# Kernel optimization log

Hardware: AMD Instinct MI355X
Metric: run time of the kernel (lower is better)

The kernel has to match this reference:

```python
import jax, jax.numpy as jnp
import numpy as np

B, S, HID = 2, 2048, 2048
H, HKV, D = 32, 8, 128


def _rope(x, cos, sin):
    # x: [B, S, n_heads, D]; cos/sin: [S, D], only first D//2 columns used.
    half = x.shape[-1] // 2
    x0, x1 = x[..., :half], x[..., half:]
    c = cos[None, :, None, :half]
    s = sin[None, :, None, :half]
    return jnp.concatenate([x0 * c - x1 * s, x0 * s + x1 * c], axis=-1)


def setup_inputs() -> dict:
    key = jax.random.key(0)
    ks = jax.random.split(key, 7)
    return {
        "hidden_states": jax.random.normal(ks[0], (B, S, HID), jnp.float32),
        "sin_table": jax.random.uniform(ks[1], (S, D), jnp.float32),
        "cos_table": jax.random.uniform(ks[2], (S, D), jnp.float32),
        "Wq": jax.random.normal(ks[3], (HID, H * D), jnp.float32) * 0.02,
        "Wk": jax.random.normal(ks[4], (HID, HKV * D), jnp.float32) * 0.02,
        "Wv": jax.random.normal(ks[5], (HID, HKV * D), jnp.float32) * 0.02,
        "Wo": jax.random.normal(ks[6], (H * D, HID), jnp.float32) * 0.02,
    }


def reference(hidden_states, sin_table, cos_table, Wq, Wk, Wv, Wo):
    b, s, _ = hidden_states.shape
    q = (hidden_states @ Wq).reshape(b, s, H, D)
    k = (hidden_states @ Wk).reshape(b, s, HKV, D)
    v = (hidden_states @ Wv).reshape(b, s, HKV, D)

    q = _rope(q, cos_table, sin_table)
    k = _rope(k, cos_table, sin_table)

    q = q.transpose(0, 2, 1, 3)  # [B, H, S, D]
    k = k.transpose(0, 2, 1, 3)  # [B, HKV, S, D]
    v = v.transpose(0, 2, 1, 3)

    g = H // HKV
    k = jnp.repeat(k, g, axis=1)  # [B, H, S, D]
    v = jnp.repeat(v, g, axis=1)

    scale = 1.0 / np.sqrt(D).astype(np.float32)
    scores = jnp.einsum("bhqd,bhkd->bhqk", q, k) * scale
    causal = jnp.tril(jnp.ones((s, s), dtype=bool))
    scores = jnp.where(causal, scores, -jnp.inf)
    attn = jax.nn.softmax(scores, axis=-1)
    out = jnp.einsum("bhqk,bhkd->bhqd", attn, v)  # [B, H, S, D]
    out = out.transpose(0, 2, 1, 3).reshape(b, s, H * D)
    return out @ Wo
```

## Files before the change

kernel.cpp:

```cpp
#include <hip/hip_runtime.h>
#include <hip/hip_bf16.h>
#include <math.h>

#define BB 2
#define SS 2048
#define HID 2048
#define NH 32
#define NKV 8
#define DD 128

typedef unsigned short u16;
typedef __attribute__((ext_vector_type(8))) short short8;
typedef __attribute__((ext_vector_type(4))) float f32x4;
typedef __attribute__((ext_vector_type(16))) float f32x16;
typedef __attribute__((ext_vector_type(4))) unsigned short us4;

__device__ __forceinline__ u16 f2bf(float f) {
    unsigned int u = __float_as_uint(f);
    u += 0x7fff + ((u >> 16) & 1);
    return (u16)(u >> 16);
}
__device__ __forceinline__ float bf2f(u16 h) {
    return __uint_as_float(((unsigned int)h) << 16);
}

#define GLOAD16(gp, lp) __builtin_amdgcn_global_load_lds(                      \
    (const __attribute__((address_space(1))) void*)(gp),                       \
    (__attribute__((address_space(3))) void*)(lp), 16, 0, 0)

#define MFMA32(a, b, c) __builtin_amdgcn_mfma_f32_32x32x16_bf16(a, b, c, 0, 0, 0)

__global__ __launch_bounds__(256) void cvt_k(const float* __restrict__ in,
                                             u16* __restrict__ out, int n8)
{
    int i = blockIdx.x * 256 + threadIdx.x;
    if (i >= n8) return;
    f32x4 a = ((const f32x4*)in)[i * 2];
    f32x4 b = ((const f32x4*)in)[i * 2 + 1];
    short8 o;
#pragma unroll
    for (int j = 0; j < 4; ++j) { o[j] = (short)f2bf(a[j]); o[4 + j] = (short)f2bf(b[j]); }
    ((short8*)out)[i] = o;
}

__global__ __launch_bounds__(256) void tw_k(const float* __restrict__ in,
                                            u16* __restrict__ out, int R, int C)
{
    __shared__ float t[32][33];
    const int tc = blockIdx.x * 32, tr = blockIdx.y * 32;
    const int r = threadIdx.x >> 3, c4 = (threadIdx.x & 7) * 4;
    f32x4 v = *(const f32x4*)(in + (size_t)(tr + r) * C + tc + c4);
#pragma unroll
    for (int j = 0; j < 4; ++j) t[r][c4 + j] = v[j];
    __syncthreads();
    us4 o;
#pragma unroll
    for (int j = 0; j < 4; ++j) o[j] = f2bf(t[c4 + j][r]);
    *(us4*)(out + (size_t)(tc + r) * R + tr + c4) = o;
}

__global__ __launch_bounds__(256) void vtr_k(const u16* __restrict__ Vb,
                                             u16* __restrict__ Vt)
{
    __shared__ u16 t[64][72];
    const int s0 = blockIdx.x * 64, d0 = blockIdx.y * 64;
    const int b = blockIdx.z >> 3, hkv = blockIdx.z & 7;
    const int tid = threadIdx.x;
    const int rr = tid >> 3, cc = (tid & 7) * 8;
#pragma unroll
    for (int it = 0; it < 2; ++it) {
        int row = rr + it * 32;
        short8 v = *(const short8*)(Vb + ((size_t)(b * SS + s0 + row) * NKV + hkv) * DD + d0 + cc);
#pragma unroll
        for (int j = 0; j < 8; ++j) t[row][cc + j] = (u16)v[j];
    }
    __syncthreads();
#pragma unroll
    for (int it = 0; it < 2; ++it) {
        int dr = rr + it * 32;
        short8 o;
#pragma unroll
        for (int j = 0; j < 8; ++j) o[j] = (short)t[cc + j][dr];
        *(short8*)(Vt + ((size_t)(b * NKV + hkv) * DD + d0 + dr) * SS + s0 + cc) = o;
    }
}

__global__ __launch_bounds__(256) void gemmqkv_k(const u16* __restrict__ A,
                                                 const u16* __restrict__ Wcat,
                                                 u16* __restrict__ Qb_,
                                                 u16* __restrict__ Kb_,
                                                 u16* __restrict__ Vt_)
{
    const int K = HID;
    const int swz = (blockIdx.x & 7) * 192 + ((int)blockIdx.x >> 3);
    const int bx = swz % 48, by = swz / 48;
    const int m0 = by * 128, n0 = bx * 128;

    __shared__ u16 Al[128 * 64];
    __shared__ u16 Bl[128 * 64];
    const int tid = threadIdx.x;
    const int lane = tid & 63, w = tid >> 6;
    const int lo = lane & 15, hi = lane >> 4;
    const int wm = w >> 1, wn = w & 1;

    const int srow = w * 32 + (lane >> 3);
    const int sslot = (lane & 7) ^ (lane >> 3);
    const u16* Asrc = A + (size_t)(m0 + srow) * K + sslot * 8;
    const u16* Bsrc = Wcat + (size_t)(n0 + srow) * K + sslot * 8;

    f32x4 acc[4][4] = {};

    for (int k0 = 0; k0 < K; k0 += 64) {
        __syncthreads();
#pragma unroll
        for (int t = 0; t < 4; ++t) {
            GLOAD16(Asrc + (size_t)t * 8 * K + k0, &Al[(w * 32 + t * 8) * 64]);
            GLOAD16(Bsrc + (size_t)t * 8 * K + k0, &Bl[(w * 32 + t * 8) * 64]);
        }
        __syncthreads();
#pragma unroll
        for (int c = 0; c < 2; ++c) {
            short8 af[4], bfv[4];
#pragma unroll
            for (int i = 0; i < 4; ++i) {
                int row = wm * 64 + i * 16 + lo;
                af[i] = *(const short8*)&Al[row * 64 + (((c * 4 + hi) ^ (lo & 7)) * 8)];
            }
#pragma unroll
            for (int j = 0; j < 4; ++j) {
                int row = wn * 64 + j * 16 + lo;
                bfv[j] = *(const short8*)&Bl[row * 64 + (((c * 4 + hi) ^ (lo & 7)) * 8)];
            }
#pragma unroll
            for (int i = 0; i < 4; ++i)
#pragma unroll
                for (int j = 0; j < 4; ++j)
                    acc[i][j] = __builtin_amdgcn_mfma_f32_16x16x32_bf16(af[i], bfv[j], acc[i][j], 0, 0, 0);
        }
    }

    if (n0 >= 5120) {
        const int cn0 = n0 - 5120;
#pragma unroll
        for (int i = 0; i < 4; ++i) {
            int gm = m0 + wm * 64 + i * 16 + hi * 4;
            int bb = gm >> 11, s = gm & (SS - 1);
#pragma unroll
            for (int j = 0; j < 4; ++j) {
                int gn = cn0 + wn * 64 + j * 16 + lo;
                int hkv = gn >> 7, d = gn & 127;
                us4 o;
#pragma unroll
                for (int r = 0; r < 4; ++r) o[r] = f2bf(acc[i][j][r]);
                *(us4*)(Vt_ + (((size_t)(bb * NKV + hkv) * DD + d) * SS + s)) = o;
            }
        }
    } else {
        u16* Cb;
        int cstride, cn0;
        if (n0 < 4096) { Cb = Qb_; cstride = NH * DD;  cn0 = n0; }
        else           { Cb = Kb_; cstride = NKV * DD; cn0 = n0 - 4096; }
#pragma unroll
        for (int i = 0; i < 4; ++i) {
            int gm = m0 + wm * 64 + i * 16 + hi * 4;
#pragma unroll
            for (int j = 0; j < 4; ++j) {
                int gn = cn0 + wn * 64 + j * 16 + lo;
#pragma unroll
                for (int r = 0; r < 4; ++r)
                    Cb[(size_t)(gm + r) * cstride + gn] = f2bf(acc[i][j][r]);
            }
        }
    }
}

template<bool C_F32>
__global__ __launch_bounds__(256) void gemm2s_k(const u16* __restrict__ A,
                                                const u16* __restrict__ Bt,
                                                void* __restrict__ Cp,
                                                int M, int N, int K, int nbx)
{
    const int cpx = (int)gridDim.x >> 3;
    const int swz = (blockIdx.x & 7) * cpx + ((int)blockIdx.x >> 3);
    const int bx = swz % nbx, by = swz / nbx;
    const int m0 = by * 128, n0 = bx * 128;

    __shared__ u16 Al[128 * 64];
    __shared__ u16 Bl[128 * 64];
    const int tid = threadIdx.x;
    const int lane = tid & 63, w = tid >> 6;
    const int lo = lane & 15, hi = lane >> 4;
    const int wm = w >> 1, wn = w & 1;

    const int srow = w * 32 + (lane >> 3);
    const int sslot = (lane & 7) ^ (lane >> 3);
    const u16* Asrc = A + (size_t)(m0 + srow) * K + sslot * 8;
    const u16* Bsrc = Bt + (size_t)(n0 + srow) * K + sslot * 8;

    f32x4 acc[4][4] = {};

    for (int k0 = 0; k0 < K; k0 += 64) {
        __syncthreads();
#pragma unroll
        for (int t = 0; t < 4; ++t) {
            GLOAD16(Asrc + (size_t)t * 8 * K + k0, &Al[(w * 32 + t * 8) * 64]);
            GLOAD16(Bsrc + (size_t)t * 8 * K + k0, &Bl[(w * 32 + t * 8) * 64]);
        }
        __syncthreads();
#pragma unroll
        for (int c = 0; c < 2; ++c) {
            short8 af[4], bfv[4];
#pragma unroll
            for (int i = 0; i < 4; ++i) {
                int row = wm * 64 + i * 16 + lo;
                af[i] = *(const short8*)&Al[row * 64 + (((c * 4 + hi) ^ (lo & 7)) * 8)];
            }
#pragma unroll
            for (int j = 0; j < 4; ++j) {
                int row = wn * 64 + j * 16 + lo;
                bfv[j] = *(const short8*)&Bl[row * 64 + (((c * 4 + hi) ^ (lo & 7)) * 8)];
            }
#pragma unroll
            for (int i = 0; i < 4; ++i)
#pragma unroll
                for (int j = 0; j < 4; ++j)
                    acc[i][j] = __builtin_amdgcn_mfma_f32_16x16x32_bf16(af[i], bfv[j], acc[i][j], 0, 0, 0);
        }
    }

#pragma unroll
    for (int i = 0; i < 4; ++i) {
        int gm = m0 + wm * 64 + i * 16 + hi * 4;
#pragma unroll
        for (int j = 0; j < 4; ++j) {
            int gn = n0 + wn * 64 + j * 16 + lo;
#pragma unroll
            for (int r = 0; r < 4; ++r) {
                if constexpr (C_F32)
                    ((float*)Cp)[(size_t)(gm + r) * N + gn] = acc[i][j][r];
                else
                    ((u16*)Cp)[(size_t)(gm + r) * N + gn] = f2bf(acc[i][j][r]);
            }
        }
    }
}

__global__ __launch_bounds__(256) void rope_k(u16* buf,
                                              const float* __restrict__ cosT,
                                              const float* __restrict__ sinT,
                                              int nheads, float scale)
{
    int idx = blockIdx.x * 256 + threadIdx.x;
    int total = BB * SS * nheads * 64;
    if (idx >= total) return;
    int d = idx & 63;
    int rem = idx >> 6;
    int hh = rem % nheads;
    int s = (rem / nheads) & (SS - 1);
    int bb = rem / (nheads * SS);
    size_t base = ((size_t)(bb * SS + s) * nheads + hh) * DD;
    float x0 = bf2f(buf[base + d]), x1 = bf2f(buf[base + d + 64]);
    float c = cosT[s * DD + d], sn = sinT[s * DD + d];
    buf[base + d]      = f2bf((x0 * c - x1 * sn) * scale);
    buf[base + d + 64] = f2bf((x0 * sn + x1 * c) * scale);
}

__device__ __forceinline__ short8 make_pa(float p0, float p1, float p2, float p3,
                                          float p4, float p5, float p6, float p7,
                                          int hi1)
{
    unsigned w0, w1, w2, w3;
    asm("v_cvt_pk_bf16_f32 %0, %1, %2" : "=v"(w0) : "v"(p0), "v"(p1));
    asm("v_cvt_pk_bf16_f32 %0, %1, %2" : "=v"(w1) : "v"(p2), "v"(p3));
    asm("v_cvt_pk_bf16_f32 %0, %1, %2" : "=v"(w2) : "v"(p4), "v"(p5));
    asm("v_cvt_pk_bf16_f32 %0, %1, %2" : "=v"(w3) : "v"(p6), "v"(p7));
    unsigned xw0 = (unsigned)__shfl_xor((int)w0, 32);
    unsigned xw1 = (unsigned)__shfl_xor((int)w1, 32);
    unsigned xw2 = (unsigned)__shfl_xor((int)w2, 32);
    unsigned xw3 = (unsigned)__shfl_xor((int)w3, 32);
    union { unsigned u[4]; short8 s; } cv;
    cv.u[0] = hi1 ? xw2 : w0;
    cv.u[1] = hi1 ? xw3 : w1;
    cv.u[2] = hi1 ? w2 : xw0;
    cv.u[3] = hi1 ? w3 : xw1;
    return cv.s;
}

__global__ __launch_bounds__(512, 2) void attn9_k(const u16* __restrict__ Qb,
                                                  const u16* __restrict__ Kb,
                                                  const u16* __restrict__ Vt,
                                                  u16* __restrict__ AO)
{
    const int wgid = blockIdx.x;
    const int k = wgid & 7;
    const int j = wgid >> 3;
    const int u = j & 31, v = j >> 5;
    const int qtb = u >> 3;
    const int qt = v ? 7 - qtb : qtb;
    const int h  = (k & 3) * 8 + (u & 7);
    const int b  = k >> 2;
    const int hkv = h >> 2;
    const int tid = threadIdx.x;
    const int w = tid >> 6, lane = tid & 63;
    const int l31 = lane & 31, hi1 = lane >> 5;
    const int qr0 = qt * 256 + w * 32;

    __shared__ u16 Kl[2][64 * 128];
    __shared__ u16 Vl[2][128 * 64];

    short8 qf[8];
    {
        const u16* qrow = Qb + ((size_t)(b * SS + qr0 + l31) * NH + h) * DD + hi1 * 8;
#pragma unroll
        for (int ks = 0; ks < 8; ++ks) qf[ks] = *(const short8*)(qrow + ks * 16);
    }

    const u16* kbase = Kb + ((size_t)b * SS * NKV + hkv) * DD;
    const u16* vbase = Vt + (size_t)(b * NKV + hkv) * DD * SS;

    f32x16 oacc[4] = {};
    float mreg = -INFINITY, lreg = 0.f;

    const int nkt = 4 * qt + 4;
    const int rk = lane >> 4, sk = lane & 15;
    const int rv = lane >> 3, sv = lane & 7;

#pragma unroll
    for (int i = 0; i < 2; ++i) {
        const int c = w * 2 + i;
        const int krow = c * 4 + rk;
        GLOAD16(kbase + (size_t)krow * (NKV * DD) + ((sk ^ (krow & 15)) * 8), &Kl[0][c * 512]);
        const int vrow = c * 8 + rv;
        GLOAD16(vbase + (size_t)vrow * SS + ((sv ^ (vrow & 7)) * 8), &Vl[0][c * 512]);
    }
    __syncthreads();

    int buf = 0;
    for (int kt = 0; kt < nkt; ++kt) {
        const int kv0 = kt * 64;
        if (kt + 1 < nkt) {
            const int kv1 = kv0 + 64;
#pragma unroll
            for (int i = 0; i < 2; ++i) {
                const int c = w * 2 + i;
                const int krow = c * 4 + rk;
                GLOAD16(kbase + (size_t)(kv1 + krow) * (NKV * DD) + ((sk ^ (krow & 15)) * 8),
                        &Kl[buf ^ 1][c * 512]);
                const int vrow = c * 8 + rv;
                GLOAD16(vbase + (size_t)vrow * SS + kv1 + ((sv ^ (vrow & 7)) * 8),
                        &Vl[buf ^ 1][c * 512]);
            }
        }

        if (kv0 <= qr0 + 31) {
            const u16* Kc = Kl[buf];
            const u16* Vc = Vl[buf];

            f32x16 s0 = {}, s1 = {};
            __builtin_amdgcn_s_setprio(1);
#pragma unroll
            for (int ks = 0; ks < 8; ++ks) {
                const int slot = (((2 * ks + hi1) ^ sk) * 8);
                short8 kf0 = *(const short8*)&Kc[l31 * 128 + slot];
                s0 = MFMA32(kf0, qf[ks], s0);
                short8 kf1 = *(const short8*)&Kc[(32 + l31) * 128 + slot];
                s1 = MFMA32(kf1, qf[ks], s1);
            }
            __builtin_amdgcn_s_setprio(0);

            const int qab = qr0 + l31;
            if (kv0 + 63 > qr0) {
#pragma unroll
                for (int r = 0; r < 16; ++r) {
                    const int off = (r & 3) + 8 * (r >> 2) + 4 * hi1;
                    if (kv0 + off > qab)      s0[r] = -INFINITY;
                    if (kv0 + 32 + off > qab) s1[r] = -INFINITY;
                }
            }
            float m0 = fmaxf(s0[0], s1[0]), m1 = fmaxf(s0[1], s1[1]);
            float m2 = fmaxf(s0[2], s1[2]), m3 = fmaxf(s0[3], s1[3]);
#pragma unroll
            for (int r = 4; r < 16; r += 4) {
                m0 = fmaxf(m0, fmaxf(s0[r],     s1[r]));
                m1 = fmaxf(m1, fmaxf(s0[r + 1], s1[r + 1]));
                m2 = fmaxf(m2, fmaxf(s0[r + 2], s1[r + 2]));
                m3 = fmaxf(m3, fmaxf(s0[r + 3], s1[r + 3]));
            }
            float mx = fmaxf(fmaxf(m0, m1), fmaxf(m2, m3));
            mx = fmaxf(mx, __shfl_xor(mx, 32));

            if (__any(mx > mreg + 8.0f)) {
                const float nm = fmaxf(mreg, mx);
                const float al = exp2f(mreg - nm);
                mreg = nm;
                lreg *= al;
#pragma unroll
                for (int r = 0; r < 16; ++r) {
                    const float ar = __shfl(al, (r & 3) + 8 * (r >> 2) + 4 * hi1);
#pragma unroll
                    for (int db = 0; db < 4; ++db) oacc[db][r] *= ar;
                }
            }

#pragma unroll
            for (int r = 0; r < 16; ++r) {
                s0[r] = exp2f(s0[r] - mreg);
                s1[r] = exp2f(s1[r] - mreg);
            }
            float sa = 0.f, sb = 0.f, sc_ = 0.f, sd = 0.f;
#pragma unroll
            for (int r = 0; r < 16; r += 4) {
                sa  += s0[r]     + s1[r];
                sb  += s0[r + 1] + s1[r + 1];
                sc_ += s0[r + 2] + s1[r + 2];
                sd  += s0[r + 3] + s1[r + 3];
            }
            lreg += (sa + sb) + (sc_ + sd);

            short8 pa0 = make_pa(s0[0], s0[1], s0[2],  s0[3],  s0[4],  s0[5],  s0[6],  s0[7],  hi1);
            short8 pa1 = make_pa(s0[8], s0[9], s0[10], s0[11], s0[12], s0[13], s0[14], s0[15], hi1);
            short8 pa2 = make_pa(s1[0], s1[1], s1[2],  s1[3],  s1[4],  s1[5],  s1[6],  s1[7],  hi1);
            short8 pa3 = make_pa(s1[8], s1[9], s1[10], s1[11], s1[12], s1[13], s1[14], s1[15], hi1);

            __builtin_amdgcn_s_setprio(1);
#pragma unroll
            for (int db = 0; db < 4; ++db) {
                const int vr = (db * 32 + l31) * 64;
                short8 vf0 = *(const short8*)&Vc[vr + (((0 + hi1) ^ sv) * 8)];
                oacc[db] = MFMA32(pa0, vf0, oacc[db]);
                short8 vf1 = *(const short8*)&Vc[vr + (((2 + hi1) ^ sv) * 8)];
                oacc[db] = MFMA32(pa1, vf1, oacc[db]);
                short8 vf2 = *(const short8*)&Vc[vr + (((4 + hi1) ^ sv) * 8)];
                oacc[db] = MFMA32(pa2, vf2, oacc[db]);
                short8 vf3 = *(const short8*)&Vc[vr + (((6 + hi1) ^ sv) * 8)];
                oacc[db] = MFMA32(pa3, vf3, oacc[db]);
            }
            __builtin_amdgcn_s_setprio(0);
        }
        __syncthreads();
        buf ^= 1;
    }

    const float lf = lreg + __shfl_xor(lreg, 32);
#pragma unroll
    for (int r = 0; r < 16; ++r) {
        const int qrw = (r & 3) + 8 * (r >> 2) + 4 * hi1;
        const float linv = 1.0f / __shfl(lf, qrw);
        u16* orow = AO + ((size_t)(b * SS + qr0 + qrw) * NH + h) * DD + l31;
#pragma unroll
        for (int db = 0; db < 4; ++db)
            orow[db * 32] = f2bf(oacc[db][r] * linv);
    }
}

template<bool A_BF16, bool C_F32>
__global__ __launch_bounds__(256) void gemm_k(const void* __restrict__ Ap,
                                              const float* __restrict__ Bp,
                                              void* __restrict__ Cp,
                                              int M, int N, int K)
{
    __shared__ u16 Asm[128 * 40];
    __shared__ u16 Bsm[128 * 40];
    const int tid  = threadIdx.x;
    const int lane = tid & 63, wid = tid >> 6;
    const int lo = lane & 15, hi = lane >> 4;
    const int wm = wid >> 1, wn = wid & 1;
    const int m0 = blockIdx.y * 128, n0 = blockIdx.x * 128;
    f32x4 acc[4][4] = {};
    const int nkt = K >> 5;
    for (int kt = 0; kt < nkt; ++kt) {
        const int k0 = kt << 5;
        __syncthreads();
        if constexpr (A_BF16) {
            const u16* A = (const u16*)Ap;
#pragma unroll
            for (int it = 0; it < 4; ++it) {
                int f = it * 256 + tid;
                int row = f >> 3, kg = (f & 7) * 4;
                us4 v = *(const us4*)(A + (size_t)(m0 + row) * K + k0 + kg);
#pragma unroll
                for (int j = 0; j < 4; ++j) Asm[row * 40 + kg + j] = v[j];
            }
        } else {
            const float* A = (const float*)Ap;
#pragma unroll
            for (int it = 0; it < 4; ++it) {
                int f = it * 256 + tid;
                int row = f >> 3, kg = (f & 7) * 4;
                f32x4 v = *(const f32x4*)(A + (size_t)(m0 + row) * K + k0 + kg);
#pragma unroll
                for (int j = 0; j < 4; ++j) Asm[row * 40 + kg + j] = f2bf(v[j]);
            }
        }
#pragma unroll
        for (int it = 0; it < 4; ++it) {
            int f = it * 256 + tid;
            int kr = f >> 5, cg = (f & 31) * 4;
            f32x4 v = *(const f32x4*)(Bp + (size_t)(k0 + kr) * N + n0 + cg);
#pragma unroll
            for (int j = 0; j < 4; ++j) Bsm[(cg + j) * 40 + kr] = f2bf(v[j]);
        }
        __syncthreads();
        short8 af[4], bfr[4];
#pragma unroll
        for (int i = 0; i < 4; ++i)
            af[i] = *(const short8*)&Asm[(wm * 64 + i * 16 + lo) * 40 + hi * 8];
#pragma unroll
        for (int j = 0; j < 4; ++j)
            bfr[j] = *(const short8*)&Bsm[(wn * 64 + j * 16 + lo) * 40 + hi * 8];
#pragma unroll
        for (int i = 0; i < 4; ++i)
#pragma unroll
            for (int j = 0; j < 4; ++j)
                acc[i][j] = __builtin_amdgcn_mfma_f32_16x16x32_bf16(af[i], bfr[j], acc[i][j], 0, 0, 0);
    }
#pragma unroll
    for (int i = 0; i < 4; ++i) {
        int gm = m0 + wm * 64 + i * 16 + hi * 4;
#pragma unroll
        for (int j = 0; j < 4; ++j) {
            int gn = n0 + wn * 64 + j * 16 + lo;
#pragma unroll
            for (int r = 0; r < 4; ++r) {
                if constexpr (C_F32)
                    ((float*)Cp)[(size_t)(gm + r) * N + gn] = acc[i][j][r];
                else
                    ((u16*)Cp)[(size_t)(gm + r) * N + gn] = f2bf(acc[i][j][r]);
            }
        }
    }
}

__global__ __launch_bounds__(64) void attn_k(const u16* __restrict__ Qb,
                                             const u16* __restrict__ Kb,
                                             const u16* __restrict__ Vb,
                                             u16* __restrict__ AO)
{
    const int blk = blockIdx.x;
    const int qt = blk & (SS / 16 - 1);
    const int h  = (blk >> 7) & (NH - 1);
    const int b  = blk >> 12;
    const int hkv = h >> 2;
    const int lane = threadIdx.x;
    const int lo = lane & 15, hi = lane >> 4;
    const int qbase = qt * 16;
    __shared__ float sc[16][32];
    __shared__ u16 vt[128 * 40];
    short8 qf[4];
    const u16* qrow = Qb + ((size_t)(b * SS + qbase + lo) * NH + h) * DD;
#pragma unroll
    for (int c = 0; c < 4; ++c) qf[c] = *(const short8*)(qrow + c * 32 + hi * 8);
    f32x4 oacc[8] = {};
    float m[4] = {-INFINITY, -INFINITY, -INFINITY, -INFINITY};
    float l[4] = {0.f, 0.f, 0.f, 0.f};
    const int nkt = (qbase + 16 + 31) >> 5;
    for (int kt = 0; kt < nkt; ++kt) {
        const int kv0 = kt << 5;
        f32x4 s0 = {}, s1 = {};
        const u16* kb0 = Kb + ((size_t)(b * SS + kv0) * NKV + hkv) * DD;
#pragma unroll
        for (int c = 0; c < 4; ++c) {
            short8 k0f = *(const short8*)(kb0 + (size_t)lo * (NKV * DD) + c * 32 + hi * 8);
            short8 k1f = *(const short8*)(kb0 + (size_t)(lo + 16) * (NKV * DD) + c * 32 + hi * 8);
            s0 = __builtin_amdgcn_mfma_f32_16x16x32_bf16(qf[c], k0f, s0, 0, 0, 0);
            s1 = __builtin_amdgcn_mfma_f32_16x16x32_bf16(qf[c], k1f, s1, 0, 0, 0);
        }
#pragma unroll
        for (int i = 0; i < 8; ++i) {
            int g = i * 64 + lane;
            int row = g >> 4, dg = (g & 15) * 8;
            short8 vv = *(const short8*)(Vb + ((size_t)(b * SS + kv0 + row) * NKV + hkv) * DD + dg);
#pragma unroll
            for (int j = 0; j < 8; ++j) vt[(dg + j) * 40 + row] = (u16)vv[j];
        }
        float alpha[4];
#pragma unroll
        for (int r = 0; r < 4; ++r) {
            int qrowi = qbase + hi * 4 + r;
            float v0 = s0[r]; if (kv0 + lo > qrowi)      v0 = -INFINITY;
            float v1 = s1[r]; if (kv0 + 16 + lo > qrowi) v1 = -INFINITY;
            float mx = fmaxf(v0, v1);
#pragma unroll
            for (int off = 1; off < 16; off <<= 1) mx = fmaxf(mx, __shfl_xor(mx, off, 64));
            float nm = fmaxf(m[r], mx);
            float a = __expf(m[r] - nm);
            v0 = __expf(v0 - nm);
            v1 = __expf(v1 - nm);
            float ps = v0 + v1;
#pragma unroll
            for (int off = 1; off < 16; off <<= 1) ps += __shfl_xor(ps, off, 64);
            l[r] = l[r] * a + ps;
            m[r] = nm;
            alpha[r] = a;
            sc[hi * 4 + r][lo] = v0;
            sc[hi * 4 + r][16 + lo] = v1;
        }
#pragma unroll
        for (int n = 0; n < 8; ++n)
#pragma unroll
            for (int r = 0; r < 4; ++r) oacc[n][r] *= alpha[r];
        __syncthreads();
        f32x4 p0 = *(const f32x4*)&sc[lo][hi * 8];
        f32x4 p1 = *(const f32x4*)&sc[lo][hi * 8 + 4];
        short8 pf;
#pragma unroll
        for (int j = 0; j < 4; ++j) {
            pf[j]     = (short)f2bf(p0[j]);
            pf[4 + j] = (short)f2bf(p1[j]);
        }
#pragma unroll
        for (int n = 0; n < 8; ++n) {
            short8 vf = *(const short8*)&vt[(n * 16 + lo) * 40 + hi * 8];
            oacc[n] = __builtin_amdgcn_mfma_f32_16x16x32_bf16(pf, vf, oacc[n], 0, 0, 0);
        }
        __syncthreads();
    }
#pragma unroll
    for (int n = 0; n < 8; ++n) {
#pragma unroll
        for (int r = 0; r < 4; ++r) {
            size_t idx = ((size_t)(b * SS + qbase + hi * 4 + r) * NH + h) * DD + n * 16 + lo;
            AO[idx] = f2bf(oacc[n][r] / l[r]);
        }
    }
}

extern "C" void kernel_launch(void* const* d_in, const int* in_sizes, int n_in,
                              void* d_out, int out_size, void* d_ws, size_t ws_size,
                              hipStream_t stream) {
    const float* hs   = (const float*)d_in[0];
    const float* sinT = (const float*)d_in[1];
    const float* cosT = (const float*)d_in[2];
    const float* Wq   = (const float*)d_in[3];
    const float* Wk   = (const float*)d_in[4];
    const float* Wv   = (const float*)d_in[5];
    const float* Wo   = (const float*)d_in[6];
    float* out = (float*)d_out;
    const int M = BB * SS;
    u16* ws = (u16*)d_ws;

    const size_t NEED = 109051904;
    if (ws_size >= NEED) {
        u16* Qb   = ws;
        u16* Kb   = ws + 16777216;
        u16* Vt   = ws + 25165824;
        u16* Wcat = ws + 29360128;
        u16* hsb  = ws + 41943040;
        u16* Wot  = Wcat;
        u16* AO   = ws + 37748736;

        cvt_k<<<4096, 256, 0, stream>>>(hs, hsb, (M * HID) / 8);
        tw_k<<<dim3(4096 / 32, 2048 / 32), 256, 0, stream>>>(Wq, Wcat, HID, NH * DD);
        tw_k<<<dim3(1024 / 32, 2048 / 32), 256, 0, stream>>>(Wk, Wcat + (size_t)4096 * 2048, HID, NKV * DD);
        tw_k<<<dim3(1024 / 32, 2048 / 32), 256, 0, stream>>>(Wv, Wcat + (size_t)5120 * 2048, HID, NKV * DD);

        gemmqkv_k<<<1536, 256, 0, stream>>>(hsb, Wcat, Qb, Kb, Vt);

        rope_k<<<(BB * SS * NH * 64 + 255) / 256, 256, 0, stream>>>(Qb, cosT, sinT, NH, 0.12751744f);
        rope_k<<<(BB * SS * NKV * 64 + 255) / 256, 256, 0, stream>>>(Kb, cosT, sinT, NKV, 1.0f);
        tw_k<<<dim3(2048 / 32, 4096 / 32), 256, 0, stream>>>(Wo, Wot, NH * DD, HID);

        attn9_k<<<SS / 256 * NH * BB, 512, 0, stream>>>(Qb, Kb, Vt, AO);

        gemm2s_k<true><<<512, 256, 0, stream>>>(AO, Wot, out, M, HID, NH * DD, HID / 128);
    } else {
        u16* Qb   = ws;
        u16* Kbuf = Qb   + (size_t)BB * SS * NH * DD;
        u16* Vbuf = Kbuf + (size_t)BB * SS * NKV * DD;
        u16* AO   = Vbuf + (size_t)BB * SS * NKV * DD;

        gemm_k<false, false><<<dim3((NH * DD) / 128, M / 128), 256, 0, stream>>>(hs, Wq, Qb, M, NH * DD, HID);
        gemm_k<false, false><<<dim3((NKV * DD) / 128, M / 128), 256, 0, stream>>>(hs, Wk, Kbuf, M, NKV * DD, HID);
        gemm_k<false, false><<<dim3((NKV * DD) / 128, M / 128), 256, 0, stream>>>(hs, Wv, Vbuf, M, NKV * DD, HID);
        rope_k<<<(BB * SS * NH * 64 + 255) / 256, 256, 0, stream>>>(Qb, cosT, sinT, NH, 0.08838834764831845f);
        rope_k<<<(BB * SS * NKV * 64 + 255) / 256, 256, 0, stream>>>(Kbuf, cosT, sinT, NKV, 1.0f);
        attn_k<<<BB * NH * (SS / 16), 64, 0, stream>>>(Qb, Kbuf, Vbuf, AO);
        gemm_k<true, true><<<dim3(HID / 128, M / 128), 256, 0, stream>>>(AO, Wo, out, M, HID, NH * DD);
    }
}
```

Baseline: 358.2 us.

## Replace QKV GEMM with 256x256-tile, 8-wave, double-buffered pipelined kernel

Replaces the 128x128 single-buffered QKV projection GEMM with a 256x256-tile kernel that uses 8 waves and two LDS stages, each holding two 128-row halves for A and B. Global-to-LDS loads for tile T+2 are issued partway through the MFMA work on tile T, using explicit vmcnt waits, barriers, sched_barrier and setprio raised around the MFMA runs. The aim is to overlap memory traffic with matrix math, raise arithmetic intensity per tile and remove the load-then-compute stall of the old loop. In exchange it uses 128 KB of LDS per block and more accumulator registers, and the hand-written wait counts and barriers are fragile. The other MFMA calls are only renamed to a macro.

```diff
diff --git a/kernel.cpp b/kernel.cpp
--- a/kernel.cpp
+++ b/kernel.cpp
@@ -29,6 +29,7 @@
     (__attribute__((address_space(3))) void*)(lp), 16, 0, 0)
 
 #define MFMA32(a, b, c) __builtin_amdgcn_mfma_f32_32x32x16_bf16(a, b, c, 0, 0, 0)
+#define MFMA16(a, b, c) __builtin_amdgcn_mfma_f32_16x16x32_bf16(a, b, c, 0, 0, 0)
 
 __global__ __launch_bounds__(256) void cvt_k(const float* __restrict__ in,
                                              u16* __restrict__ out, int n8)
@@ -85,15 +86,168 @@
     }
 }
 
-__global__ __launch_bounds__(256) void gemmqkv_k(const u16* __restrict__ A,
-                                                 const u16* __restrict__ Wcat,
-                                                 u16* __restrict__ Qb_,
-                                                 u16* __restrict__ Kb_,
-                                                 u16* __restrict__ Vt_)
+__global__ __launch_bounds__(512, 2) void gemm8qkv_k(const u16* __restrict__ A,
+                                                     const u16* __restrict__ Bt,
+                                                     u16* __restrict__ Qb_,
+                                                     u16* __restrict__ Kb_,
+                                                     u16* __restrict__ Vt_)
 {
     const int K = HID;
-    const int swz = (blockIdx.x & 7) * 192 + ((int)blockIdx.x >> 3);
-    const int bx = swz % 48, by = swz / 48;
+    const int k8 = blockIdx.x & 7;
+    const int j  = (int)blockIdx.x >> 3;
+    const int bx = j >> 1, by = k8 * 2 + (j & 1);
+    const int m0 = by * 256, n0 = bx * 256;
+
+    __shared__ u16 Asl[4][128 * 64];
+    __shared__ u16 Bsl[4][128 * 64];
+
+    const int tid = threadIdx.x;
+    const int w = tid >> 6, lane = tid & 63;
+    const int wm = w >> 2, wn = w & 3;
+    const int lo = lane & 15, hi = lane >> 4;
+    const int brow0 = (wn & 1) * 64;
+
+    const int srow8 = lane >> 3;
+    const int skk = ((lane & 7) ^ srow8) * 8;
+    const u16* As = A + (size_t)(m0 + w * 16 + srow8) * K + skk;
+    const u16* Bs = Bt + (size_t)(n0 + w * 16 + srow8) * K + skk;
+
+#define SA8(slot, half, kof) do {                                                        \
+    GLOAD16(As + (size_t)((half) * 128) * K + (kof), &Asl[slot][(w * 16) * 64]);         \
+    GLOAD16(As + (size_t)((half) * 128 + 8) * K + (kof), &Asl[slot][(w * 16 + 8) * 64]); \
+  } while (0)
+#define SB8(slot, half, kof) do {                                                        \
+    GLOAD16(Bs + (size_t)((half) * 128) * K + (kof), &Bsl[slot][(w * 16) * 64]);         \
+    GLOAD16(Bs + (size_t)((half) * 128 + 8) * K + (kof), &Bsl[slot][(w * 16 + 8) * 64]); \
+  } while (0)
+#define PHASE_END() do {                                       \
+    asm volatile("s_waitcnt lgkmcnt(0)" ::: "memory");         \
+    __builtin_amdgcn_sched_barrier(0);                         \
+    __builtin_amdgcn_s_barrier();                              \
+  } while (0)
+
+    f32x4 acc[8][4] = {};
+    const int nt = K >> 6;
+
+    SA8(0, 0, 0);  SA8(1, 1, 0);  SB8(0, 0, 0);  SB8(1, 1, 0);
+    SA8(2, 0, 64); SA8(3, 1, 64); SB8(2, 0, 64); SB8(3, 1, 64);
+    asm volatile("s_waitcnt vmcnt(8)" ::: "memory");
+    __builtin_amdgcn_s_barrier();
+
+#define TILE8(P, T) do {                                                                 \
+    const u16* Apan = Asl[(P) * 2 + wm];                                                 \
+    const u16* Bpan = Bsl[(P) * 2 + (wn >> 1)];                                          \
+    short8 afr[2][8]; short8 bfr[2][4];                                                  \
+                    \
+    _Pragma("unroll") for (int c = 0; c < 2; ++c) {                                      \
+      _Pragma("unroll") for (int i = 0; i < 4; ++i)                                      \
+        afr[c][i] = *(const short8*)&Apan[(i * 16 + lo) * 64 + (((c * 4 + hi) ^ (lo & 7)) * 8)]; \
+      _Pragma("unroll") for (int jj = 0; jj < 2; ++jj)                                   \
+        bfr[c][jj] = *(const short8*)&Bpan[(brow0 + jj * 16 + lo) * 64 + (((c * 4 + hi) ^ (lo & 7)) * 8)]; \
+    }                                                                                    \
+    __builtin_amdgcn_s_setprio(1);                                                       \
+    _Pragma("unroll") for (int i = 0; i < 4; ++i)                                        \
+      _Pragma("unroll") for (int jj = 0; jj < 2; ++jj) {                                 \
+        acc[i][jj] = MFMA16(afr[0][i], bfr[0][jj], acc[i][jj]);                          \
+        acc[i][jj] = MFMA16(afr[1][i], bfr[1][jj], acc[i][jj]);                          \
+      }                                                                                  \
+    __builtin_amdgcn_s_setprio(0);                                                       \
+    PHASE_END();                                                                         \
+                          \
+    _Pragma("unroll") for (int c = 0; c < 2; ++c) {                                      \
+      _Pragma("unroll") for (int i = 4; i < 8; ++i)                                      \
+        afr[c][i] = *(const short8*)&Apan[(i * 16 + lo) * 64 + (((c * 4 + hi) ^ (lo & 7)) * 8)]; \
+      _Pragma("unroll") for (int jj = 2; jj < 4; ++jj)                                   \
+        bfr[c][jj] = *(const short8*)&Bpan[(brow0 + jj * 16 + lo) * 64 + (((c * 4 + hi) ^ (lo & 7)) * 8)]; \
+    }                                                                                    \
+    __builtin_amdgcn_s_setprio(1);                                                       \
+    _Pragma("unroll") for (int i = 0; i < 4; ++i)                                        \
+      _Pragma("unroll") for (int jj = 2; jj < 4; ++jj) {                                 \
+        acc[i][jj] = MFMA16(afr[0][i], bfr[0][jj], acc[i][jj]);                          \
+        acc[i][jj] = MFMA16(afr[1][i], bfr[1][jj], acc[i][jj]);                          \
+      }                                                                                  \
+    __builtin_amdgcn_s_setprio(0);                                                       \
+    PHASE_END();                                                                         \
+                          \
+    __builtin_amdgcn_s_setprio(1);                                                       \
+    _Pragma("unroll") for (int i = 4; i < 8; ++i)                                        \
+      _Pragma("unroll") for (int jj = 0; jj < 2; ++jj) {                                 \
+        acc[i][jj] = MFMA16(afr[0][i], bfr[0][jj], acc[i][jj]);                          \
+        acc[i][jj] = MFMA16(afr[1][i], bfr[1][jj], acc[i][jj]);                          \
+      }                                                                                  \
+    __builtin_amdgcn_s_setprio(0);                                                       \
+    if ((T) + 2 < nt) {                                                                  \
+      SA8((P) * 2 + 0, 0, ((T) + 2) * 64); SA8((P) * 2 + 1, 1, ((T) + 2) * 64);          \
+    }                                                                                    \
+    PHASE_END();                                                                         \
+           \
+    __builtin_amdgcn_s_setprio(1);                                                       \
+    _Pragma("unroll") for (int i = 4; i < 8; ++i)                                        \
+      _Pragma("unroll") for (int jj = 2; jj < 4; ++jj) {                                 \
+        acc[i][jj] = MFMA16(afr[0][i], bfr[0][jj], acc[i][jj]);                          \
+        acc[i][jj] = MFMA16(afr[1][i], bfr[1][jj], acc[i][jj]);                          \
+      }                                                                                  \
+    __builtin_amdgcn_s_setprio(0);                                                       \
+    if ((T) + 2 < nt) {                                                                  \
+      SB8((P) * 2 + 0, 0, ((T) + 2) * 64); SB8((P) * 2 + 1, 1, ((T) + 2) * 64);          \
+      asm volatile("s_waitcnt vmcnt(8)" ::: "memory");                                   \
+    } else {                                                                             \
+      asm volatile("s_waitcnt vmcnt(0)" ::: "memory");                                   \
+    }                                                                                    \
+    asm volatile("s_waitcnt lgkmcnt(0)" ::: "memory");                                   \
+    __builtin_amdgcn_sched_barrier(0);                                                   \
+    __builtin_amdgcn_s_barrier();                                                        \
+  } while (0)
+
+    for (int T = 0; T < nt; T += 2) {
+        TILE8(0, T);
+        TILE8(1, T + 1);
+    }
+#undef TILE8
+
+    if (n0 >= 5120) {
+#pragma unroll
+        for (int i = 0; i < 8; ++i) {
+            int gm = m0 + wm * 128 + i * 16 + hi * 4;
+            int bb = gm >> 11, s = gm & (SS - 1);
+#pragma unroll
+            for (int jj = 0; jj < 4; ++jj) {
+                int gn = (n0 - 5120) + wn * 64 + jj * 16 + lo;
+                int hkv = gn >> 7, d = gn & 127;
+                us4 o;
+#pragma unroll
+                for (int r = 0; r < 4; ++r) o[r] = f2bf(acc[i][jj][r]);
+                *(us4*)(Vt_ + (((size_t)(bb * NKV + hkv) * DD + d) * SS + s)) = o;
+            }
+        }
+    } else {
+        u16* Cb;
+        int cstride, cn0;
+        if (n0 < 4096) { Cb = Qb_; cstride = NH * DD;  cn0 = n0; }
+        else           { Cb = Kb_; cstride = NKV * DD; cn0 = n0 - 4096; }
+#pragma unroll
+        for (int i = 0; i < 8; ++i) {
+            int gm = m0 + wm * 128 + i * 16 + hi * 4;
+#pragma unroll
+            for (int jj = 0; jj < 4; ++jj) {
+                int gn = cn0 + wn * 64 + jj * 16 + lo;
+#pragma unroll
+                for (int r = 0; r < 4; ++r)
+                    Cb[(size_t)(gm + r) * cstride + gn] = f2bf(acc[i][jj][r]);
+            }
+        }
+    }
+}
+
+template<bool C_F32>
+__global__ __launch_bounds__(256) void gemm2s_k(const u16* __restrict__ A,
+                                                const u16* __restrict__ Bt,
+                                                void* __restrict__ Cp,
+                                                int M, int N, int K, int nbx)
+{
+    const int cpx = (int)gridDim.x >> 3;
+    const int swz = (blockIdx.x & 7) * cpx + ((int)blockIdx.x >> 3);
+    const int bx = swz % nbx, by = swz / nbx;
     const int m0 = by * 128, n0 = bx * 128;
 
     __shared__ u16 Al[128 * 64];
@@ -106,7 +260,7 @@
     const int srow = w * 32 + (lane >> 3);
     const int sslot = (lane & 7) ^ (lane >> 3);
     const u16* Asrc = A + (size_t)(m0 + srow) * K + sslot * 8;
-    const u16* Bsrc = Wcat + (size_t)(n0 + srow) * K + sslot * 8;
+    const u16* Bsrc = Bt + (size_t)(n0 + srow) * K + sslot * 8;
 
     f32x4 acc[4][4] = {};
 
@@ -135,96 +289,7 @@
             for (int i = 0; i < 4; ++i)
 #pragma unroll
                 for (int j = 0; j < 4; ++j)
-                    acc[i][j] = __builtin_amdgcn_mfma_f32_16x16x32_bf16(af[i], bfv[j], acc[i][j], 0, 0, 0);
-        }
-    }
-
-    if (n0 >= 5120) {
-        const int cn0 = n0 - 5120;
-#pragma unroll
-        for (int i = 0; i < 4; ++i) {
-            int gm = m0 + wm * 64 + i * 16 + hi * 4;
-            int bb = gm >> 11, s = gm & (SS - 1);
-#pragma unroll
-            for (int j = 0; j < 4; ++j) {
-                int gn = cn0 + wn * 64 + j * 16 + lo;
-                int hkv = gn >> 7, d = gn & 127;
-                us4 o;
-#pragma unroll
-                for (int r = 0; r < 4; ++r) o[r] = f2bf(acc[i][j][r]);
-                *(us4*)(Vt_ + (((size_t)(bb * NKV + hkv) * DD + d) * SS + s)) = o;
-            }
-        }
-    } else {
-        u16* Cb;
-        int cstride, cn0;
-        if (n0 < 4096) { Cb = Qb_; cstride = NH * DD;  cn0 = n0; }
-        else           { Cb = Kb_; cstride = NKV * DD; cn0 = n0 - 4096; }
-#pragma unroll
-        for (int i = 0; i < 4; ++i) {
-            int gm = m0 + wm * 64 + i * 16 + hi * 4;
-#pragma unroll
-            for (int j = 0; j < 4; ++j) {
-                int gn = cn0 + wn * 64 + j * 16 + lo;
-#pragma unroll
-                for (int r = 0; r < 4; ++r)
-                    Cb[(size_t)(gm + r) * cstride + gn] = f2bf(acc[i][j][r]);
-            }
-        }
-    }
-}
-
-template<bool C_F32>
-__global__ __launch_bounds__(256) void gemm2s_k(const u16* __restrict__ A,
-                                                const u16* __restrict__ Bt,
-                                                void* __restrict__ Cp,
-                                                int M, int N, int K, int nbx)
-{
-    const int cpx = (int)gridDim.x >> 3;
-    const int swz = (blockIdx.x & 7) * cpx + ((int)blockIdx.x >> 3);
-    const int bx = swz % nbx, by = swz / nbx;
-    const int m0 = by * 128, n0 = bx * 128;
-
-    __shared__ u16 Al[128 * 64];
-    __shared__ u16 Bl[128 * 64];
-    const int tid = threadIdx.x;
-    const int lane = tid & 63, w = tid >> 6;
-    const int lo = lane & 15, hi = lane >> 4;
-    const int wm = w >> 1, wn = w & 1;
-
-    const int srow = w * 32 + (lane >> 3);
-    const int sslot = (lane & 7) ^ (lane >> 3);
-    const u16* Asrc = A + (size_t)(m0 + srow) * K + sslot * 8;
-    const u16* Bsrc = Bt + (size_t)(n0 + srow) * K + sslot * 8;
-
-    f32x4 acc[4][4] = {};
-
-    for (int k0 = 0; k0 < K; k0 += 64) {
-        __syncthreads();
-#pragma unroll
-        for (int t = 0; t < 4; ++t) {
-            GLOAD16(Asrc + (size_t)t * 8 * K + k0, &Al[(w * 32 + t * 8) * 64]);
-            GLOAD16(Bsrc + (size_t)t * 8 * K + k0, &Bl[(w * 32 + t * 8) * 64]);
-        }
-        __syncthreads();
-#pragma unroll
-        for (int c = 0; c < 2; ++c) {
-            short8 af[4], bfv[4];
-#pragma unroll
-            for (int i = 0; i < 4; ++i) {
-                int row = wm * 64 + i * 16 + lo;
-                af[i] = *(const short8*)&Al[row * 64 + (((c * 4 + hi) ^ (lo & 7)) * 8)];
-            }
-#pragma unroll
-            for (int j = 0; j < 4; ++j) {
-                int row = wn * 64 + j * 16 + lo;
-                bfv[j] = *(const short8*)&Bl[row * 64 + (((c * 4 + hi) ^ (lo & 7)) * 8)];
-            }
-#pragma unroll
-            for (int i = 0; i < 4; ++i)
-#pragma unroll
-                for (int j = 0; j < 4; ++j)
-                    acc[i][j] = __builtin_amdgcn_mfma_f32_16x16x32_bf16(af[i], bfv[j], acc[i][j], 0, 0, 0);
+                    acc[i][j] = MFMA16(af[i], bfv[j], acc[i][j]);
         }
     }
 
@@ -512,7 +577,7 @@
         for (int i = 0; i < 4; ++i)
 #pragma unroll
             for (int j = 0; j < 4; ++j)
-                acc[i][j] = __builtin_amdgcn_mfma_f32_16x16x32_bf16(af[i], bfr[j], acc[i][j], 0, 0, 0);
+                acc[i][j] = MFMA16(af[i], bfr[j], acc[i][j]);
     }
 #pragma unroll
     for (int i = 0; i < 4; ++i) {
@@ -562,8 +627,8 @@
         for (int c = 0; c < 4; ++c) {
             short8 k0f = *(const short8*)(kb0 + (size_t)lo * (NKV * DD) + c * 32 + hi * 8);
             short8 k1f = *(const short8*)(kb0 + (size_t)(lo + 16) * (NKV * DD) + c * 32 + hi * 8);
-            s0 = __builtin_amdgcn_mfma_f32_16x16x32_bf16(qf[c], k0f, s0, 0, 0, 0);
-            s1 = __builtin_amdgcn_mfma_f32_16x16x32_bf16(qf[c], k1f, s1, 0, 0, 0);
+            s0 = MFMA16(qf[c], k0f, s0);
+            s1 = MFMA16(qf[c], k1f, s1);
         }
 #pragma unroll
         for (int i = 0; i < 8; ++i) {
@@ -611,7 +676,7 @@
 #pragma unroll
         for (int n = 0; n < 8; ++n) {
             short8 vf = *(const short8*)&vt[(n * 16 + lo) * 40 + hi * 8];
-            oacc[n] = __builtin_amdgcn_mfma_f32_16x16x32_bf16(pf, vf, oacc[n], 0, 0, 0);
+            oacc[n] = MFMA16(pf, vf, oacc[n]);
         }
         __syncthreads();
     }
@@ -654,7 +719,7 @@
         tw_k<<<dim3(1024 / 32, 2048 / 32), 256, 0, stream>>>(Wk, Wcat + (size_t)4096 * 2048, HID, NKV * DD);
         tw_k<<<dim3(1024 / 32, 2048 / 32), 256, 0, stream>>>(Wv, Wcat + (size_t)5120 * 2048, HID, NKV * DD);
 
-        gemmqkv_k<<<1536, 256, 0, stream>>>(hsb, Wcat, Qb, Kb, Vt);
+        gemm8qkv_k<<<384, 512, 0, stream>>>(hsb, Wcat, Qb, Kb, Vt);
 
         rope_k<<<(BB * SS * NH * 64 + 255) / 256, 256, 0, stream>>>(Qb, cosT, sinT, NH, 0.12751744f);
         rope_k<<<(BB * SS * NKV * 64 + 255) / 256, 256, 0, stream>>>(Kb, cosT, sinT, NKV, 1.0f);
```

New measurement: 357.3 us. About the same (-0.2%).
